# Performance work log

Measured on AMD Instinct MI355X. Metric: run time of the kernel, lower is better.

Reference implementation:

```python
import jax, jax.numpy as jnp
import numpy as np

EPS = 1e-5

def _layernorm(x, g, b):
    mu = jnp.mean(x, axis=-1, keepdims=True)
    var = jnp.mean(jnp.square(x - mu), axis=-1, keepdims=True)
    return (x - mu) * jax.lax.rsqrt(var + EPS) * g + b

def setup_inputs() -> dict:
    key = jax.random.key(0)
    ks = jax.random.split(key, 5)
    F_, H, D = 1024, 16, 64
    B, N = 4, 2048
    s = lambda k, shp, fan: jax.random.normal(k, shp, jnp.float32) * (fan ** -0.5)
    return {
        "x": jax.random.normal(ks[0], (B, N, F_), jnp.float32),
        "Wq": s(ks[1], (H * D, F_), F_),
        "Wkv": s(ks[2], (2 * H * D, F_), F_),
        "Wo": s(ks[3], (F_, H * D), H * D),
        "ln_g": jnp.ones((F_,), jnp.float32),
        "ln_b": jnp.zeros((F_,), jnp.float32),
        "lnc_g": jnp.ones((F_,), jnp.float32),
        "lnc_b": jnp.zeros((F_,), jnp.float32),
    }

def reference(x, Wq, Wkv, Wo, ln_g, ln_b, lnc_g, lnc_b):
    H, D = 16, 64
    scale = D ** -0.5
    skip = x
    xn = _layernorm(x, ln_g, ln_b)          # query path norm
    cn = _layernorm(x, lnc_g, lnc_b)        # context (self) norm
    B, N, _ = x.shape
    q = jnp.einsum('bnf,ef->bne', xn, Wq)   # [B,N,H*D]
    kv = jnp.einsum('bnf,ef->bne', cn, Wkv) # [B,N,2*H*D]
    k, v = jnp.split(kv, 2, axis=-1)
    tohd = lambda t: t.reshape(B, N, H, D).transpose(0, 2, 1, 3)  # b h n d
    q, k, v = tohd(q), tohd(k), tohd(v)
    sim = jnp.einsum('bhnd,bhmd->bhnm', q, k) * scale
    attn = jax.nn.softmax(sim, axis=-1)
    out = jnp.einsum('bhnm,bhmd->bhnd', attn, v)
    out = out.transpose(0, 2, 1, 3).reshape(B, N, H * D)
    out = jnp.einsum('bne,fe->bnf', out, Wo)
    return skip + out
```

## Files before the change

kernel.cpp:

```cpp
#include <hip/hip_runtime.h>
#include <hip/hip_bf16.h>
#include <stdint.h>

typedef __bf16 bf16;
typedef __bf16 bf16x8 __attribute__((ext_vector_type(8)));
typedef __bf16 bf16x4 __attribute__((ext_vector_type(4)));
typedef float f32x4 __attribute__((ext_vector_type(4)));
typedef unsigned u32x2 __attribute__((ext_vector_type(2)));

#define F_DIM 1024
#define NSEQ  2048
#define NB    4
#define NH    16
#define HD    64
#define MROWS (NB * NSEQ)
#define LOG2E 1.44269504088896340736f

__device__ __forceinline__ void gload_lds16(const void* g, void* l) {
    __builtin_amdgcn_global_load_lds(
        (__attribute__((address_space(1))) void*)g,
        (__attribute__((address_space(3))) void*)l,
        16, 0, 0);
}

__device__ __forceinline__ unsigned lds_addr(const void* p) {
    return (unsigned)(size_t)(__attribute__((address_space(3))) const void*)p;
}

__global__ __launch_bounds__(256) void ln2_kernel(
    const float* __restrict__ x,
    const float* __restrict__ g1, const float* __restrict__ b1,
    const float* __restrict__ g2, const float* __restrict__ b2,
    bf16* __restrict__ xn, bf16* __restrict__ cn)
{
    const int row = blockIdx.x;
    const int t = threadIdx.x;
    float4 v = reinterpret_cast<const float4*>(x + (size_t)row * F_DIM)[t];
    float s  = v.x + v.y + v.z + v.w;
    float ss = v.x * v.x + v.y * v.y + v.z * v.z + v.w * v.w;
#pragma unroll
    for (int m = 1; m < 64; m <<= 1) {
        s  += __shfl_xor(s, m);
        ss += __shfl_xor(ss, m);
    }
    __shared__ float red[8];
    const int w = t >> 6;
    if ((t & 63) == 0) { red[w] = s; red[4 + w] = ss; }
    __syncthreads();
    s  = red[0] + red[1] + red[2] + red[3];
    ss = red[4] + red[5] + red[6] + red[7];
    const float mu  = s * (1.0f / F_DIM);
    const float var = fmaxf(ss * (1.0f / F_DIM) - mu * mu, 0.0f);
    const float rs  = rsqrtf(var + 1e-5f);

    float4 G1 = reinterpret_cast<const float4*>(g1)[t];
    float4 B1 = reinterpret_cast<const float4*>(b1)[t];
    float4 G2 = reinterpret_cast<const float4*>(g2)[t];
    float4 B2 = reinterpret_cast<const float4*>(b2)[t];
    const float h0 = (v.x - mu) * rs, h1 = (v.y - mu) * rs;
    const float h2 = (v.z - mu) * rs, h3 = (v.w - mu) * rs;
    bf16x4 o1 = { (bf16)(h0 * G1.x + B1.x), (bf16)(h1 * G1.y + B1.y),
                  (bf16)(h2 * G1.z + B1.z), (bf16)(h3 * G1.w + B1.w) };
    bf16x4 o2 = { (bf16)(h0 * G2.x + B2.x), (bf16)(h1 * G2.y + B2.y),
                  (bf16)(h2 * G2.z + B2.z), (bf16)(h3 * G2.w + B2.w) };
    *reinterpret_cast<bf16x4*>(xn + (size_t)row * F_DIM + t * 4) = o1;
    *reinterpret_cast<bf16x4*>(cn + (size_t)row * F_DIM + t * 4) = o2;
}

__global__ __launch_bounds__(256) void cvt_kernel(
    const float* __restrict__ src, bf16* __restrict__ dst, int n4)
{
    int i = blockIdx.x * 256 + threadIdx.x;
    if (i < n4) {
        float4 v = reinterpret_cast<const float4*>(src)[i];
        bf16x4 o = { (bf16)v.x, (bf16)v.y, (bf16)v.z, (bf16)v.w };
        reinterpret_cast<bf16x4*>(dst)[i] = o;
    }
}

template <int EPI>
__global__ __launch_bounds__(256, 2) void gemm_bt(
    const bf16* __restrict__ A, const bf16* __restrict__ B,
    bf16* __restrict__ Cb, float* __restrict__ Cf,
    const float* __restrict__ skip, int M, int N, int K, float oscale)
{
    __shared__ bf16 As[128 * 32];
    __shared__ bf16 Bs[128 * 32];
    const int t = threadIdx.x;
    const int lane = t & 63;
    const int w = t >> 6;
    const int wr = w >> 1, wc = w & 1;

    int flat = blockIdx.y * gridDim.x + blockIdx.x;
    const int nwg = gridDim.x * gridDim.y;
    if ((nwg & 7) == 0)
        flat = (flat & 7) * (nwg >> 3) + (flat >> 3);
    const int bm = (flat / gridDim.x) * 128;
    const int bn = (flat % gridDim.x) * 128;

    const int r = lane & 15;
    const int kg = (lane >> 4) * 8;

    f32x4 acc[4][4];
#pragma unroll
    for (int i = 0; i < 4; i++)
#pragma unroll
        for (int j = 0; j < 4; j++) acc[i][j] = (f32x4){0.f, 0.f, 0.f, 0.f};

    const int c0 = t, c1 = 256 + t;
    const size_t aoff0 = (size_t)(bm + (c0 >> 2)) * K + (c0 & 3) * 8;
    const size_t aoff1 = (size_t)(bm + (c1 >> 2)) * K + (c1 & 3) * 8;
    const size_t boff0 = (size_t)(bn + (c0 >> 2)) * K + (c0 & 3) * 8;
    const size_t boff1 = (size_t)(bn + (c1 >> 2)) * K + (c1 & 3) * 8;
    bf16* lA0 = As + (size_t)(0 * 256 + w * 64) * 8;
    bf16* lA1 = As + (size_t)(1 * 256 + w * 64) * 8;
    bf16* lB0 = Bs + (size_t)(0 * 256 + w * 64) * 8;
    bf16* lB1 = Bs + (size_t)(1 * 256 + w * 64) * 8;

    for (int kt = 0; kt < K; kt += 32) {
        gload_lds16(A + aoff0 + kt, lA0);
        gload_lds16(A + aoff1 + kt, lA1);
        gload_lds16(B + boff0 + kt, lB0);
        gload_lds16(B + boff1 + kt, lB1);
        __syncthreads();
        bf16x8 af[4], bfr[4];
#pragma unroll
        for (int mi = 0; mi < 4; mi++)
            af[mi] = *(const bf16x8*)(As + (wr * 64 + mi * 16 + r) * 32 + kg);
#pragma unroll
        for (int ni = 0; ni < 4; ni++)
            bfr[ni] = *(const bf16x8*)(Bs + (wc * 64 + ni * 16 + r) * 32 + kg);
#pragma unroll
        for (int mi = 0; mi < 4; mi++)
#pragma unroll
            for (int ni = 0; ni < 4; ni++)
                acc[mi][ni] = __builtin_amdgcn_mfma_f32_16x16x32_bf16(
                    af[mi], bfr[ni], acc[mi][ni], 0, 0, 0);
        __syncthreads();
    }

    const int g = lane >> 4;
#pragma unroll
    for (int mi = 0; mi < 4; mi++) {
#pragma unroll
        for (int ni = 0; ni < 4; ni++) {
            const int col = bn + wc * 64 + ni * 16 + r;
#pragma unroll
            for (int j = 0; j < 4; j++) {
                const int row = bm + wr * 64 + mi * 16 + g * 4 + j;
                const float vv = acc[mi][ni][j];
                if (EPI == 0) {
                    Cb[(size_t)row * N + col] = (bf16)(vv * oscale);
                } else {
                    Cf[(size_t)row * N + col] = vv + skip[(size_t)row * N + col];
                }
            }
        }
    }
}

__global__ __launch_bounds__(256, 4) void attn_kernel(
    const bf16* __restrict__ q, const bf16* __restrict__ kvp,
    bf16* __restrict__ o)
{
    __shared__ __align__(16) bf16 Ks[64 * 64];
    __shared__ __align__(16) bf16 Vs[64 * 64];
    __shared__ __align__(16) bf16 Ps[4][16 * 72];

    const int bid = blockIdx.x;
    const int idx = (bid & 7) * 256 + (bid >> 3);
    const int bh = idx >> 5;
    const int qt = idx & 31;
    const int b = bh >> 4, h = bh & 15;

    const int t = threadIdx.x, lane = t & 63, w = t >> 6;
    const int r = lane & 15, g = lane >> 4;

    const size_t rowq = (size_t)b * NSEQ;

    size_t ksrc[2], vsrc[2];
#pragma unroll
    for (int c = 0; c < 2; c++) {
        const int p = c * 256 + t;
        const int krow = p >> 3;
        const int kcol = (p & 7) ^ (krow & 7);
        ksrc[c] = (size_t)(rowq + krow) * (2 * F_DIM) + h * HD + kcol * 8;
        const int kvb = p >> 5, dblk = (p >> 3) & 3;
        const int kvl = (p & 7) >> 1, d8 = p & 1;
        vsrc[c] = (size_t)(rowq + kvb * 4 + kvl) * (2 * F_DIM) + F_DIM + h * HD
                  + dblk * 16 + d8 * 8;
    }

    const int q0 = qt * 64 + w * 16;
    bf16x8 qf[2];
#pragma unroll
    for (int kk = 0; kk < 2; kk++)
        qf[kk] = *(const bf16x8*)(q + (rowq + q0 + r) * F_DIM + h * HD + kk * 32 + g * 8);

    f32x4 oacc[4];
#pragma unroll
    for (int i = 0; i < 4; i++) oacc[i] = (f32x4){0.f, 0.f, 0.f, 0.f};
    float m_r = -1e30f, l_r = 0.f;

    const unsigned va = lds_addr(Vs) + (unsigned)(g * 1024 + r * 8);

    bf16x8 kpre0 = *(const bf16x8*)(kvp + ksrc[0]);
    bf16x8 kpre1 = *(const bf16x8*)(kvp + ksrc[1]);
    bf16x8 vpre0 = *(const bf16x8*)(kvp + vsrc[0]);
    bf16x8 vpre1 = *(const bf16x8*)(kvp + vsrc[1]);

    for (int kv0 = 0; kv0 < NSEQ; kv0 += 64) {
        asm volatile("s_barrier" ::: "memory");

        *(bf16x8*)&Ks[t * 8]         = kpre0;
        *(bf16x8*)&Ks[(256 + t) * 8] = kpre1;
        *(bf16x8*)&Vs[t * 8]         = vpre0;
        *(bf16x8*)&Vs[(256 + t) * 8] = vpre1;

        if (kv0 + 64 < NSEQ) {
            const size_t koff = (size_t)(kv0 + 64) * (2 * F_DIM);
            kpre0 = *(const bf16x8*)(kvp + ksrc[0] + koff);
            kpre1 = *(const bf16x8*)(kvp + ksrc[1] + koff);
            vpre0 = *(const bf16x8*)(kvp + vsrc[0] + koff);
            vpre1 = *(const bf16x8*)(kvp + vsrc[1] + koff);
        }

        asm volatile("s_waitcnt lgkmcnt(0)\n\ts_barrier" ::: "memory");

        f32x4 s4[4];
#pragma unroll
        for (int nt = 0; nt < 4; nt++) s4[nt] = (f32x4){0.f, 0.f, 0.f, 0.f};
        __builtin_amdgcn_s_setprio(1);
#pragma unroll
        for (int kk = 0; kk < 2; kk++) {
#pragma unroll
            for (int nt = 0; nt < 4; nt++) {
                const unsigned lb = (unsigned)((nt * 16 + r) * 128 + kk * 64 + g * 16)
                                    ^ (unsigned)((r & 7) << 4);
                bf16x8 kf = *(const bf16x8*)((const char*)Ks + lb);
                s4[nt] = __builtin_amdgcn_mfma_f32_16x16x32_bf16(kf, qf[kk], s4[nt], 0, 0, 0);
            }
        }
        __builtin_amdgcn_s_setprio(0);

        float mx = fmaxf(fmaxf(fmaxf(s4[0][0], s4[0][1]), fmaxf(s4[0][2], s4[0][3])),
                         fmaxf(fmaxf(s4[1][0], s4[1][1]), fmaxf(s4[1][2], s4[1][3])));
        mx = fmaxf(mx, fmaxf(fmaxf(fmaxf(s4[2][0], s4[2][1]), fmaxf(s4[2][2], s4[2][3])),
                             fmaxf(fmaxf(s4[3][0], s4[3][1]), fmaxf(s4[3][2], s4[3][3]))));
        mx = fmaxf(mx, __shfl_xor(mx, 16));
        mx = fmaxf(mx, __shfl_xor(mx, 32));
        if (!__all(mx <= m_r + 8.0f)) {
            const float mnew = fmaxf(m_r, mx);
            const float alpha = exp2f(m_r - mnew);
            l_r *= alpha;
#pragma unroll
            for (int j = 0; j < 4; j++) {
                const float aj = __shfl(alpha, g * 4 + j);
#pragma unroll
                for (int ntd = 0; ntd < 4; ntd++) oacc[ntd][j] *= aj;
            }
            m_r = mnew;
        }
        float ps = 0.f;
#pragma unroll
        for (int nt = 0; nt < 4; nt++)
#pragma unroll
            for (int j = 0; j < 4; j++) {
                const float pp = exp2f(s4[nt][j] - m_r);
                s4[nt][j] = pp;
                ps += pp;
            }
        ps += __shfl_xor(ps, 16);
        ps += __shfl_xor(ps, 32);
        l_r += ps;

#pragma unroll
        for (int nt = 0; nt < 4; nt++) {
            bf16x4 pb = { (bf16)s4[nt][0], (bf16)s4[nt][1],
                          (bf16)s4[nt][2], (bf16)s4[nt][3] };
            *(bf16x4*)&Ps[w][r * 72 + nt * 16 + g * 4] = pb;
        }

        bf16x8 pf[2];
#pragma unroll
        for (int kk = 0; kk < 2; kk++)
            pf[kk] = *(const bf16x8*)&Ps[w][r * 72 + kk * 32 + g * 8];

        u32x2 vt[4][2][2];
#pragma unroll
        for (int ntd = 0; ntd < 4; ntd++)
#pragma unroll
            for (int kk = 0; kk < 2; kk++) {
                const unsigned a = va + (unsigned)(kk * 4096 + ntd * 128);
                asm volatile("ds_read_b64_tr_b16 %0, %2\n\t"
                             "ds_read_b64_tr_b16 %1, %2 offset:512"
                             : "=&v"(vt[ntd][kk][0]), "=&v"(vt[ntd][kk][1])
                             : "v"(a));
            }
        asm volatile("s_waitcnt lgkmcnt(0)" ::: "memory");
        __builtin_amdgcn_sched_barrier(0);

        __builtin_amdgcn_s_setprio(1);
#pragma unroll
        for (int ntd = 0; ntd < 4; ntd++)
#pragma unroll
            for (int kk = 0; kk < 2; kk++) {
                union { u32x2 h[2]; bf16x8 v; } u;
                u.h[0] = vt[ntd][kk][0];
                u.h[1] = vt[ntd][kk][1];
                oacc[ntd] = __builtin_amdgcn_mfma_f32_16x16x32_bf16(pf[kk], u.v, oacc[ntd], 0, 0, 0);
            }
        __builtin_amdgcn_s_setprio(0);
    }

    float rl[4];
#pragma unroll
    for (int j = 0; j < 4; j++) {
        const float lj = __shfl(l_r, g * 4 + j);
        rl[j] = 1.0f / lj;
    }
#pragma unroll
    for (int ntd = 0; ntd < 4; ntd++)
#pragma unroll
        for (int j = 0; j < 4; j++) {
            const int row = q0 + g * 4 + j;
            o[(rowq + row) * F_DIM + h * HD + ntd * 16 + r] =
                (bf16)(oacc[ntd][j] * rl[j]);
        }
}

extern "C" void kernel_launch(void* const* d_in, const int* in_sizes, int n_in,
                              void* d_out, int out_size, void* d_ws, size_t ws_size,
                              hipStream_t stream)
{
    const float* x     = (const float*)d_in[0];
    const float* Wq    = (const float*)d_in[1];
    const float* Wkv   = (const float*)d_in[2];
    const float* Wo    = (const float*)d_in[3];
    const float* ln_g  = (const float*)d_in[4];
    const float* ln_b  = (const float*)d_in[5];
    const float* lnc_g = (const float*)d_in[6];
    const float* lnc_b = (const float*)d_in[7];
    float* out = (float*)d_out;

    bf16* xn   = (bf16*)d_ws;
    bf16* cn   = xn  + (size_t)MROWS * F_DIM;
    bf16* qb   = cn  + (size_t)MROWS * F_DIM;
    bf16* kvb  = qb  + (size_t)MROWS * F_DIM;
    bf16* wqb  = kvb + (size_t)MROWS * 2 * F_DIM;
    bf16* wkvb = wqb + (size_t)F_DIM * F_DIM;
    bf16* wob  = wkvb + (size_t)2 * F_DIM * F_DIM;
    bf16* ao   = xn;

    ln2_kernel<<<dim3(MROWS), dim3(256), 0, stream>>>(x, ln_g, ln_b, lnc_g, lnc_b, xn, cn);

    cvt_kernel<<<dim3((F_DIM * F_DIM / 4 + 255) / 256), dim3(256), 0, stream>>>(Wq, wqb, F_DIM * F_DIM / 4);
    cvt_kernel<<<dim3((2 * F_DIM * F_DIM / 4 + 255) / 256), dim3(256), 0, stream>>>(Wkv, wkvb, 2 * F_DIM * F_DIM / 4);
    cvt_kernel<<<dim3((F_DIM * F_DIM / 4 + 255) / 256), dim3(256), 0, stream>>>(Wo, wob, F_DIM * F_DIM / 4);

    gemm_bt<0><<<dim3(F_DIM / 128, MROWS / 128), dim3(256), 0, stream>>>(
        xn, wqb, qb, nullptr, nullptr, MROWS, F_DIM, F_DIM, 0.125f * LOG2E);
    gemm_bt<0><<<dim3(2 * F_DIM / 128, MROWS / 128), dim3(256), 0, stream>>>(
        cn, wkvb, kvb, nullptr, nullptr, MROWS, 2 * F_DIM, F_DIM, 1.0f);
    attn_kernel<<<dim3(NSEQ / 64 * NB * NH), dim3(256), 0, stream>>>(qb, kvb, ao);
    gemm_bt<1><<<dim3(F_DIM / 128, MROWS / 128), dim3(256), 0, stream>>>(
        ao, wob, nullptr, out, x, MROWS, F_DIM, F_DIM, 1.0f);
}
```

Before: 262.5 us.

## Double KV tile to 128, load via global_load_lds, pipeline PV LDS reads

Raises the attention KV tile from 64 to 128 rows and loads K/V straight into LDS with global_load_lds instead of register prefetch plus ds_write. The PV loop is software-pipelined, reading the next P and V fragments while the current MFMAs run. exp2f becomes raw v_exp_f32 and the bf16 packing uses v_cvt_pk_bf16_f32. The cost is that the register prefetch is gone, so global load latency is exposed at each tile start, and occupancy drops from 4 to 3 blocks because of the larger LDS footprint.

Result: faster. 235.2 us (-10.4%).

```diff
diff --git a/kernel.cpp b/kernel.cpp
--- a/kernel.cpp
+++ b/kernel.cpp
@@ -25,6 +25,18 @@
 
 __device__ __forceinline__ unsigned lds_addr(const void* p) {
     return (unsigned)(size_t)(__attribute__((address_space(3))) const void*)p;
+}
+
+__device__ __forceinline__ float exp2_fast(float x) {
+    float r;
+    asm("v_exp_f32 %0, %1" : "=v"(r) : "v"(x));
+    return r;
+}
+
+__device__ __forceinline__ unsigned cvtpk_bf16(float lo, float hi) {
+    unsigned r;
+    asm("v_cvt_pk_bf16_f32 %0, %1, %2" : "=v"(r) : "v"(lo), "v"(hi));
+    return r;
 }
 
 __global__ __launch_bounds__(256) void ln2_kernel(
@@ -159,13 +171,13 @@
     }
 }
 
-__global__ __launch_bounds__(256, 4) void attn_kernel(
+__global__ __launch_bounds__(256, 3) void attn_kernel(
     const bf16* __restrict__ q, const bf16* __restrict__ kvp,
     bf16* __restrict__ o)
 {
-    __shared__ __align__(16) bf16 Ks[64 * 64];
-    __shared__ __align__(16) bf16 Vs[64 * 64];
-    __shared__ __align__(16) bf16 Ps[4][16 * 72];
+    __shared__ __align__(16) bf16 Ks[128 * 64];
+    __shared__ __align__(16) bf16 Vs[128 * 64];
+    __shared__ __align__(16) bf16 Ps[4][16 * 136];
 
     const int bid = blockIdx.x;
     const int idx = (bid & 7) * 256 + (bid >> 3);
@@ -178,9 +190,9 @@
 
     const size_t rowq = (size_t)b * NSEQ;
 
-    size_t ksrc[2], vsrc[2];
-#pragma unroll
-    for (int c = 0; c < 2; c++) {
+    size_t ksrc[4], vsrc[4];
+#pragma unroll
+    for (int c = 0; c < 4; c++) {
         const int p = c * 256 + t;
         const int krow = p >> 3;
         const int kcol = (p & 7) ^ (krow & 7);
@@ -202,39 +214,28 @@
     for (int i = 0; i < 4; i++) oacc[i] = (f32x4){0.f, 0.f, 0.f, 0.f};
     float m_r = -1e30f, l_r = 0.f;
 
-    const unsigned va = lds_addr(Vs) + (unsigned)(g * 1024 + r * 8);
-
-    bf16x8 kpre0 = *(const bf16x8*)(kvp + ksrc[0]);
-    bf16x8 kpre1 = *(const bf16x8*)(kvp + ksrc[1]);
-    bf16x8 vpre0 = *(const bf16x8*)(kvp + vsrc[0]);
-    bf16x8 vpre1 = *(const bf16x8*)(kvp + vsrc[1]);
-
-    for (int kv0 = 0; kv0 < NSEQ; kv0 += 64) {
+    const unsigned va    = lds_addr(Vs) + (unsigned)(g * 1024 + r * 8);
+    const unsigned pbase = lds_addr(&Ps[w][0]) + (unsigned)((r * 136 + g * 8) * 2);
+
+    for (int kv0 = 0; kv0 < NSEQ; kv0 += 128) {
         asm volatile("s_barrier" ::: "memory");
-
-        *(bf16x8*)&Ks[t * 8]         = kpre0;
-        *(bf16x8*)&Ks[(256 + t) * 8] = kpre1;
-        *(bf16x8*)&Vs[t * 8]         = vpre0;
-        *(bf16x8*)&Vs[(256 + t) * 8] = vpre1;
-
-        if (kv0 + 64 < NSEQ) {
-            const size_t koff = (size_t)(kv0 + 64) * (2 * F_DIM);
-            kpre0 = *(const bf16x8*)(kvp + ksrc[0] + koff);
-            kpre1 = *(const bf16x8*)(kvp + ksrc[1] + koff);
-            vpre0 = *(const bf16x8*)(kvp + vsrc[0] + koff);
-            vpre1 = *(const bf16x8*)(kvp + vsrc[1] + koff);
-        }
-
-        asm volatile("s_waitcnt lgkmcnt(0)\n\ts_barrier" ::: "memory");
-
-        f32x4 s4[4];
-#pragma unroll
-        for (int nt = 0; nt < 4; nt++) s4[nt] = (f32x4){0.f, 0.f, 0.f, 0.f};
+        const size_t koff = (size_t)kv0 * (2 * F_DIM);
+#pragma unroll
+        for (int c = 0; c < 4; c++)
+            gload_lds16(kvp + ksrc[c] + koff, Ks + (size_t)(c * 256 + (t & ~63)) * 8);
+#pragma unroll
+        for (int c = 0; c < 4; c++)
+            gload_lds16(kvp + vsrc[c] + koff, Vs + (size_t)(c * 256 + (t & ~63)) * 8);
+        asm volatile("s_waitcnt vmcnt(0)\n\ts_barrier" ::: "memory");
+
+        f32x4 s4[8];
+#pragma unroll
+        for (int nt = 0; nt < 8; nt++) s4[nt] = (f32x4){0.f, 0.f, 0.f, 0.f};
         __builtin_amdgcn_s_setprio(1);
 #pragma unroll
         for (int kk = 0; kk < 2; kk++) {
 #pragma unroll
-            for (int nt = 0; nt < 4; nt++) {
+            for (int nt = 0; nt < 8; nt++) {
                 const unsigned lb = (unsigned)((nt * 16 + r) * 128 + kk * 64 + g * 16)
                                     ^ (unsigned)((r & 7) << 4);
                 bf16x8 kf = *(const bf16x8*)((const char*)Ks + lb);
@@ -243,15 +244,16 @@
         }
         __builtin_amdgcn_s_setprio(0);
 
-        float mx = fmaxf(fmaxf(fmaxf(s4[0][0], s4[0][1]), fmaxf(s4[0][2], s4[0][3])),
-                         fmaxf(fmaxf(s4[1][0], s4[1][1]), fmaxf(s4[1][2], s4[1][3])));
-        mx = fmaxf(mx, fmaxf(fmaxf(fmaxf(s4[2][0], s4[2][1]), fmaxf(s4[2][2], s4[2][3])),
-                             fmaxf(fmaxf(s4[3][0], s4[3][1]), fmaxf(s4[3][2], s4[3][3]))));
+        float mx = s4[0][0];
+#pragma unroll
+        for (int nt = 0; nt < 8; nt++)
+#pragma unroll
+            for (int j = 0; j < 4; j++) mx = fmaxf(mx, s4[nt][j]);
         mx = fmaxf(mx, __shfl_xor(mx, 16));
         mx = fmaxf(mx, __shfl_xor(mx, 32));
         if (!__all(mx <= m_r + 8.0f)) {
             const float mnew = fmaxf(m_r, mx);
-            const float alpha = exp2f(m_r - mnew);
+            const float alpha = exp2_fast(m_r - mnew);
             l_r *= alpha;
 #pragma unroll
             for (int j = 0; j < 4; j++) {
@@ -263,10 +265,10 @@
         }
         float ps = 0.f;
 #pragma unroll
-        for (int nt = 0; nt < 4; nt++)
+        for (int nt = 0; nt < 8; nt++)
 #pragma unroll
             for (int j = 0; j < 4; j++) {
-                const float pp = exp2f(s4[nt][j] - m_r);
+                const float pp = exp2_fast(s4[nt][j] - m_r);
                 s4[nt][j] = pp;
                 ps += pp;
             }
@@ -275,42 +277,56 @@
         l_r += ps;
 
 #pragma unroll
-        for (int nt = 0; nt < 4; nt++) {
-            bf16x4 pb = { (bf16)s4[nt][0], (bf16)s4[nt][1],
-                          (bf16)s4[nt][2], (bf16)s4[nt][3] };
-            *(bf16x4*)&Ps[w][r * 72 + nt * 16 + g * 4] = pb;
-        }
+        for (int nt = 0; nt < 8; nt++) {
+            u32x2 pw = { cvtpk_bf16(s4[nt][0], s4[nt][1]),
+                         cvtpk_bf16(s4[nt][2], s4[nt][3]) };
+            *(u32x2*)&Ps[w][r * 136 + nt * 16 + g * 4] = pw;
+        }
+        asm volatile("s_waitcnt lgkmcnt(0)" ::: "memory");
 
         bf16x8 pf[2];
-#pragma unroll
-        for (int kk = 0; kk < 2; kk++)
-            pf[kk] = *(const bf16x8*)&Ps[w][r * 72 + kk * 32 + g * 8];
-
-        u32x2 vt[4][2][2];
-#pragma unroll
-        for (int ntd = 0; ntd < 4; ntd++)
-#pragma unroll
-            for (int kk = 0; kk < 2; kk++) {
-                const unsigned a = va + (unsigned)(kk * 4096 + ntd * 128);
+        u32x2 vt[2][4][2];
+        {
+            const unsigned pa = pbase + 0 * 64;
+            asm volatile("ds_read_b128 %0, %1" : "=v"(pf[0]) : "v"(pa));
+#pragma unroll
+            for (int ntd = 0; ntd < 4; ntd++) {
+                const unsigned a = va + (unsigned)(0 * 4096 + ntd * 128);
                 asm volatile("ds_read_b64_tr_b16 %0, %2\n\t"
                              "ds_read_b64_tr_b16 %1, %2 offset:512"
-                             : "=&v"(vt[ntd][kk][0]), "=&v"(vt[ntd][kk][1])
+                             : "=&v"(vt[0][ntd][0]), "=&v"(vt[0][ntd][1])
                              : "v"(a));
             }
-        asm volatile("s_waitcnt lgkmcnt(0)" ::: "memory");
-        __builtin_amdgcn_sched_barrier(0);
-
-        __builtin_amdgcn_s_setprio(1);
-#pragma unroll
-        for (int ntd = 0; ntd < 4; ntd++)
-#pragma unroll
-            for (int kk = 0; kk < 2; kk++) {
+        }
+#pragma unroll
+        for (int kk = 0; kk < 4; kk++) {
+            const int cu = kk & 1, nx = cu ^ 1;
+            if (kk < 3) {
+                const unsigned pa = pbase + (unsigned)((kk + 1) * 64);
+                asm volatile("ds_read_b128 %0, %1" : "=v"(pf[nx]) : "v"(pa));
+#pragma unroll
+                for (int ntd = 0; ntd < 4; ntd++) {
+                    const unsigned a = va + (unsigned)((kk + 1) * 4096 + ntd * 128);
+                    asm volatile("ds_read_b64_tr_b16 %0, %2\n\t"
+                                 "ds_read_b64_tr_b16 %1, %2 offset:512"
+                                 : "=&v"(vt[nx][ntd][0]), "=&v"(vt[nx][ntd][1])
+                                 : "v"(a));
+                }
+                asm volatile("s_waitcnt lgkmcnt(9)" ::: "memory");
+            } else {
+                asm volatile("s_waitcnt lgkmcnt(0)" ::: "memory");
+            }
+            __builtin_amdgcn_sched_barrier(0);
+            __builtin_amdgcn_s_setprio(1);
+#pragma unroll
+            for (int ntd = 0; ntd < 4; ntd++) {
                 union { u32x2 h[2]; bf16x8 v; } u;
-                u.h[0] = vt[ntd][kk][0];
-                u.h[1] = vt[ntd][kk][1];
-                oacc[ntd] = __builtin_amdgcn_mfma_f32_16x16x32_bf16(pf[kk], u.v, oacc[ntd], 0, 0, 0);
-            }
-        __builtin_amdgcn_s_setprio(0);
+                u.h[0] = vt[cu][ntd][0];
+                u.h[1] = vt[cu][ntd][1];
+                oacc[ntd] = __builtin_amdgcn_mfma_f32_16x16x32_bf16(pf[cu], u.v, oacc[ntd], 0, 0, 0);
+            }
+            __builtin_amdgcn_s_setprio(0);
+        }
     }
 
     float rl[4];
```

## Enlarge attention blocks to 128 queries and load K/V directly to LDS

Applied to the files above, without the earlier changes.

The attention kernel now uses 512 threads (8 waves) per block, each block covering 128 query rows, so each K/V tile staged in LDS is reused by twice as many waves. K/V tiles are loaded with global_load_lds straight into shared memory instead of register prefetch plus LDS stores. This drops the software double-buffering, so every iteration waits on vmcnt(0) and global latency is exposed. The change also uses raw v_exp_f32 and v_cvt_pk_bf16_f32, and reads P with an explicit ds_read_b128 ordered by kk.

Result: slower. 281.5 us (+7.2%).

```diff
diff --git a/kernel.cpp b/kernel.cpp
--- a/kernel.cpp
+++ b/kernel.cpp
@@ -25,6 +25,18 @@
 
 __device__ __forceinline__ unsigned lds_addr(const void* p) {
     return (unsigned)(size_t)(__attribute__((address_space(3))) const void*)p;
+}
+
+__device__ __forceinline__ float exp2_fast(float x) {
+    float r;
+    asm("v_exp_f32 %0, %1" : "=v"(r) : "v"(x));
+    return r;
+}
+
+__device__ __forceinline__ unsigned cvtpk_bf16(float lo, float hi) {
+    unsigned r;
+    asm("v_cvt_pk_bf16_f32 %0, %1, %2" : "=v"(r) : "v"(lo), "v"(hi));
+    return r;
 }
 
 __global__ __launch_bounds__(256) void ln2_kernel(
@@ -159,18 +171,18 @@
     }
 }
 
-__global__ __launch_bounds__(256, 4) void attn_kernel(
+__global__ __launch_bounds__(512, 6) void attn_kernel(
     const bf16* __restrict__ q, const bf16* __restrict__ kvp,
     bf16* __restrict__ o)
 {
     __shared__ __align__(16) bf16 Ks[64 * 64];
     __shared__ __align__(16) bf16 Vs[64 * 64];
-    __shared__ __align__(16) bf16 Ps[4][16 * 72];
+    __shared__ __align__(16) bf16 Ps[8][16 * 72];
 
     const int bid = blockIdx.x;
-    const int idx = (bid & 7) * 256 + (bid >> 3);
-    const int bh = idx >> 5;
-    const int qt = idx & 31;
+    const int idx = (bid & 7) * 128 + (bid >> 3);
+    const int bh = idx >> 4;
+    const int qt = idx & 15;
     const int b = bh >> 4, h = bh & 15;
 
     const int t = threadIdx.x, lane = t & 63, w = t >> 6;
@@ -178,20 +190,18 @@
 
     const size_t rowq = (size_t)b * NSEQ;
 
-    size_t ksrc[2], vsrc[2];
-#pragma unroll
-    for (int c = 0; c < 2; c++) {
-        const int p = c * 256 + t;
-        const int krow = p >> 3;
-        const int kcol = (p & 7) ^ (krow & 7);
-        ksrc[c] = (size_t)(rowq + krow) * (2 * F_DIM) + h * HD + kcol * 8;
-        const int kvb = p >> 5, dblk = (p >> 3) & 3;
-        const int kvl = (p & 7) >> 1, d8 = p & 1;
-        vsrc[c] = (size_t)(rowq + kvb * 4 + kvl) * (2 * F_DIM) + F_DIM + h * HD
-                  + dblk * 16 + d8 * 8;
-    }
-
-    const int q0 = qt * 64 + w * 16;
+    const int p = t;
+    const int krow = p >> 3;
+    const int kcol = (p & 7) ^ (krow & 7);
+    const size_t ksrc = (size_t)(rowq + krow) * (2 * F_DIM) + h * HD + kcol * 8;
+    const int kvb = p >> 5, dblk = (p >> 3) & 3;
+    const int kvl = (p & 7) >> 1, d8 = p & 1;
+    const size_t vsrc = (size_t)(rowq + kvb * 4 + kvl) * (2 * F_DIM) + F_DIM + h * HD
+                        + dblk * 16 + d8 * 8;
+    bf16* kdst = Ks + (size_t)(t & ~63) * 8;
+    bf16* vdst = Vs + (size_t)(t & ~63) * 8;
+
+    const int q0 = qt * 128 + w * 16;
     bf16x8 qf[2];
 #pragma unroll
     for (int kk = 0; kk < 2; kk++)
@@ -202,30 +212,15 @@
     for (int i = 0; i < 4; i++) oacc[i] = (f32x4){0.f, 0.f, 0.f, 0.f};
     float m_r = -1e30f, l_r = 0.f;
 
-    const unsigned va = lds_addr(Vs) + (unsigned)(g * 1024 + r * 8);
-
-    bf16x8 kpre0 = *(const bf16x8*)(kvp + ksrc[0]);
-    bf16x8 kpre1 = *(const bf16x8*)(kvp + ksrc[1]);
-    bf16x8 vpre0 = *(const bf16x8*)(kvp + vsrc[0]);
-    bf16x8 vpre1 = *(const bf16x8*)(kvp + vsrc[1]);
+    const unsigned va    = lds_addr(Vs) + (unsigned)(g * 1024 + r * 8);
+    const unsigned pbase = lds_addr(&Ps[w][0]) + (unsigned)((r * 72 + g * 8) * 2);
 
     for (int kv0 = 0; kv0 < NSEQ; kv0 += 64) {
         asm volatile("s_barrier" ::: "memory");
-
-        *(bf16x8*)&Ks[t * 8]         = kpre0;
-        *(bf16x8*)&Ks[(256 + t) * 8] = kpre1;
-        *(bf16x8*)&Vs[t * 8]         = vpre0;
-        *(bf16x8*)&Vs[(256 + t) * 8] = vpre1;
-
-        if (kv0 + 64 < NSEQ) {
-            const size_t koff = (size_t)(kv0 + 64) * (2 * F_DIM);
-            kpre0 = *(const bf16x8*)(kvp + ksrc[0] + koff);
-            kpre1 = *(const bf16x8*)(kvp + ksrc[1] + koff);
-            vpre0 = *(const bf16x8*)(kvp + vsrc[0] + koff);
-            vpre1 = *(const bf16x8*)(kvp + vsrc[1] + koff);
-        }
-
-        asm volatile("s_waitcnt lgkmcnt(0)\n\ts_barrier" ::: "memory");
+        const size_t koff = (size_t)kv0 * (2 * F_DIM);
+        gload_lds16(kvp + ksrc + koff, kdst);
+        gload_lds16(kvp + vsrc + koff, vdst);
+        asm volatile("s_waitcnt vmcnt(0)\n\ts_barrier" ::: "memory");
 
         f32x4 s4[4];
 #pragma unroll
@@ -243,15 +238,16 @@
         }
         __builtin_amdgcn_s_setprio(0);
 
-        float mx = fmaxf(fmaxf(fmaxf(s4[0][0], s4[0][1]), fmaxf(s4[0][2], s4[0][3])),
-                         fmaxf(fmaxf(s4[1][0], s4[1][1]), fmaxf(s4[1][2], s4[1][3])));
-        mx = fmaxf(mx, fmaxf(fmaxf(fmaxf(s4[2][0], s4[2][1]), fmaxf(s4[2][2], s4[2][3])),
-                             fmaxf(fmaxf(s4[3][0], s4[3][1]), fmaxf(s4[3][2], s4[3][3]))));
+        float mx = s4[0][0];
+#pragma unroll
+        for (int nt = 0; nt < 4; nt++)
+#pragma unroll
+            for (int j = 0; j < 4; j++) mx = fmaxf(mx, s4[nt][j]);
         mx = fmaxf(mx, __shfl_xor(mx, 16));
         mx = fmaxf(mx, __shfl_xor(mx, 32));
         if (!__all(mx <= m_r + 8.0f)) {
             const float mnew = fmaxf(m_r, mx);
-            const float alpha = exp2f(m_r - mnew);
+            const float alpha = exp2_fast(m_r - mnew);
             l_r *= alpha;
 #pragma unroll
             for (int j = 0; j < 4; j++) {
@@ -266,7 +262,7 @@
         for (int nt = 0; nt < 4; nt++)
 #pragma unroll
             for (int j = 0; j < 4; j++) {
-                const float pp = exp2f(s4[nt][j] - m_r);
+                const float pp = exp2_fast(s4[nt][j] - m_r);
                 s4[nt][j] = pp;
                 ps += pp;
             }
@@ -276,38 +272,37 @@
 
 #pragma unroll
         for (int nt = 0; nt < 4; nt++) {
-            bf16x4 pb = { (bf16)s4[nt][0], (bf16)s4[nt][1],
-                          (bf16)s4[nt][2], (bf16)s4[nt][3] };
-            *(bf16x4*)&Ps[w][r * 72 + nt * 16 + g * 4] = pb;
+            u32x2 pw = { cvtpk_bf16(s4[nt][0], s4[nt][1]),
+                         cvtpk_bf16(s4[nt][2], s4[nt][3]) };
+            *(u32x2*)&Ps[w][r * 72 + nt * 16 + g * 4] = pw;
         }
 
         bf16x8 pf[2];
-#pragma unroll
-        for (int kk = 0; kk < 2; kk++)
-            pf[kk] = *(const bf16x8*)&Ps[w][r * 72 + kk * 32 + g * 8];
-
-        u32x2 vt[4][2][2];
-#pragma unroll
-        for (int ntd = 0; ntd < 4; ntd++)
-#pragma unroll
-            for (int kk = 0; kk < 2; kk++) {
+        u32x2 vt[2][4][2];
+#pragma unroll
+        for (int kk = 0; kk < 2; kk++) {
+            const unsigned pa = pbase + (unsigned)(kk * 64);
+            asm volatile("ds_read_b128 %0, %1" : "=v"(pf[kk]) : "v"(pa));
+#pragma unroll
+            for (int ntd = 0; ntd < 4; ntd++) {
                 const unsigned a = va + (unsigned)(kk * 4096 + ntd * 128);
                 asm volatile("ds_read_b64_tr_b16 %0, %2\n\t"
                              "ds_read_b64_tr_b16 %1, %2 offset:512"
-                             : "=&v"(vt[ntd][kk][0]), "=&v"(vt[ntd][kk][1])
+                             : "=&v"(vt[kk][ntd][0]), "=&v"(vt[kk][ntd][1])
                              : "v"(a));
             }
+        }
         asm volatile("s_waitcnt lgkmcnt(0)" ::: "memory");
         __builtin_amdgcn_sched_barrier(0);
 
         __builtin_amdgcn_s_setprio(1);
 #pragma unroll
-        for (int ntd = 0; ntd < 4; ntd++)
-#pragma unroll
-            for (int kk = 0; kk < 2; kk++) {
+        for (int kk = 0; kk < 2; kk++)
+#pragma unroll
+            for (int ntd = 0; ntd < 4; ntd++) {
                 union { u32x2 h[2]; bf16x8 v; } u;
-                u.h[0] = vt[ntd][kk][0];
-                u.h[1] = vt[ntd][kk][1];
+                u.h[0] = vt[kk][ntd][0];
+                u.h[1] = vt[kk][ntd][1];
                 oacc[ntd] = __builtin_amdgcn_mfma_f32_16x16x32_bf16(pf[kk], u.v, oacc[ntd], 0, 0, 0);
             }
         __builtin_amdgcn_s_setprio(0);
@@ -362,7 +357,7 @@
         xn, wqb, qb, nullptr, nullptr, MROWS, F_DIM, F_DIM, 0.125f * LOG2E);
     gemm_bt<0><<<dim3(2 * F_DIM / 128, MROWS / 128), dim3(256), 0, stream>>>(
         cn, wkvb, kvb, nullptr, nullptr, MROWS, 2 * F_DIM, F_DIM, 1.0f);
-    attn_kernel<<<dim3(NSEQ / 64 * NB * NH), dim3(256), 0, stream>>>(qb, kvb, ao);
+    attn_kernel<<<dim3(NSEQ / 128 * NB * NH), dim3(512), 0, stream>>>(qb, kvb, ao);
     gemm_bt<1><<<dim3(F_DIM / 128, MROWS / 128), dim3(256), 0, stream>>>(
         ao, wob, nullptr, out, x, MROWS, F_DIM, F_DIM, 1.0f);
 }
```
